# Performance work log

Measured on AMD Instinct MI355X. Metric: run time of the kernel, lower is better.

The kernel has to match this reference:

```python
import jax, jax.numpy as jnp
import numpy as np

B, N, DH, DG, HID, K_STEPS, CURV = 256, 2048, 128, 256, 256, 2, 1.0
SC = CURV ** 0.5
SCALE = 1.0 / (DH ** 0.5)
LN_EPS = 1e-5


def _artanh(x):
    return jnp.arctanh(jnp.clip(x, -1.0 + 1e-5, 1.0 - 1e-5))


def logmap0(x, sc=SC):
    n = jnp.maximum(jnp.linalg.norm(x, axis=-1, keepdims=True), 1e-7)
    return x * (_artanh(sc * n) / (sc * n))


def expmap0(v, sc=SC):
    n = jnp.maximum(jnp.linalg.norm(v, axis=-1, keepdims=True), 1e-7)
    return v * (jnp.tanh(sc * n) / (sc * n))


def setup_inputs() -> dict:
    key = jax.random.key(0)
    ks = jax.random.split(key, 16)

    def lin(k, out_d, in_d):
        return (jax.random.normal(k, (out_d, in_d), jnp.float32) * (in_d ** -0.5))

    demo_hyp = expmap0(0.1 * jax.random.normal(ks[0], (B, N, DH), jnp.float32))
    rho_g = jax.random.normal(ks[1], (B, DG), jnp.float32)
    return {
        "demo_hyp": demo_hyp,
        "rho_g": rho_g,
        "seed_g_w": lin(ks[2], DH, DG),
        "seed_g_b": jnp.zeros((DH,), jnp.float32),
        "seed_d_w": lin(ks[3], DH, DH),
        "pool_wq_w": lin(ks[4], DH, DH),
        "pool_wk_w": lin(ks[5], DH, DH),
        "pool_wv_w": lin(ks[6], DH, DH),
        "q_u_w": lin(ks[7], DH, DH),
        "q_g_w": lin(ks[8], DH, DG),
        "q_g_b": jnp.zeros((DH,), jnp.float32),
        "kv_w": lin(ks[9], DH, DH),
        "mlp_w1": lin(ks[10], HID, DH),
        "mlp_b1": jnp.zeros((HID,), jnp.float32),
        "mlp_w2": lin(ks[11], DH, HID),
        "mlp_b2": jnp.zeros((DH,), jnp.float32),
        "ln_g": jnp.ones((DH,), jnp.float32),
        "ln_b": jnp.zeros((DH,), jnp.float32),
    }


def reference(demo_hyp, rho_g, seed_g_w, seed_g_b, seed_d_w,
              pool_wq_w, pool_wk_w, pool_wv_w, q_u_w, q_g_w, q_g_b,
              kv_w, mlp_w1, mlp_b1, mlp_w2, mlp_b2, ln_g, ln_b):
    demo_tan = logmap0(demo_hyp)                       # (B,N,Dh)

    # seed: attention-pool demos with rho_g query
    q_seed = rho_g @ seed_g_w.T + seed_g_b             # (B,Dh)
    qk = q_seed @ pool_wq_w.T                          # (B,Dh)
    Kp = demo_tan @ pool_wk_w.T                        # (B,N,Dh)
    a = jax.nn.softmax(jnp.einsum('bd,bnd->bn', qk, Kp) * SCALE, axis=-1)
    Vp = demo_tan @ pool_wv_w.T
    pooled = jnp.einsum('bn,bnd->bd', a, Vp)           # (B,Dh)
    u = expmap0(q_seed + pooled @ seed_d_w.T)

    for _ in range(K_STEPS):
        u_tan = logmap0(u)
        mu = jnp.mean(u_tan, axis=-1, keepdims=True)
        var = jnp.var(u_tan, axis=-1, keepdims=True)
        u_tan = (u_tan - mu) * jax.lax.rsqrt(var + LN_EPS) * ln_g + ln_b
        q = u_tan @ q_u_w.T + rho_g @ q_g_w.T + q_g_b
        Kmat = demo_tan @ kv_w.T                       # keys == values
        att = jax.nn.softmax(jnp.einsum('bd,bnd->bn', q, Kmat) * SCALE, axis=-1)
        delta = jnp.einsum('bn,bnd->bd', att, Kmat)
        upd = jax.nn.gelu(delta @ mlp_w1.T + mlp_b1, approximate=False) @ mlp_w2.T + mlp_b2
        u = expmap0(u_tan + upd)
    return u
```

## Files before the change

kernel.cpp:

```cpp
#include <hip/hip_runtime.h>
#include <hip/hip_fp16.h>
#include <cstddef>
#include <cstdint>

#define B 256
#define N 2048
#define DH 128
#define DG 256
#define HID 256
#define WAVES 16
#define TPB (WAVES * 64)
#define RPI (WAVES * 8)
#define KIT (N / RPI)
#define SCALE 0.08838834764831845f
#define LN_EPS 1e-5f
#define TAN_NORM_MAX 6.2f


__device__ __forceinline__ float artanh_clip(float a) {
  a = fminf(a, 1.0f - 1e-5f);
  return 0.5f * __logf((1.0f + a) / (1.0f - a));
}

__device__ __forceinline__ float logmap_scale(float n2) {
  float nc = fmaxf(sqrtf(n2), 1e-7f);
  return artanh_clip(nc) / nc;
}

__device__ __forceinline__ float row16_sum(float x) {
  x += __int_as_float(__builtin_amdgcn_update_dpp(0, __float_as_int(x), 0x128, 0xF, 0xF, true));
  x += __int_as_float(__builtin_amdgcn_update_dpp(0, __float_as_int(x), 0x124, 0xF, 0xF, true));
  x += __int_as_float(__builtin_amdgcn_update_dpp(0, __float_as_int(x), 0x122, 0xF, 0xF, true));
  x += __int_as_float(__builtin_amdgcn_update_dpp(0, __float_as_int(x), 0x121, 0xF, 0xF, true));
  return x;
}

__device__ __forceinline__ float wave_allsum(float v) {
#pragma unroll
  for (int m = 1; m < 64; m <<= 1) v += __shfl_xor(v, m);
  return v;
}

__device__ __forceinline__ float dot128(const float* __restrict__ wrow,
                                        const float* __restrict__ x) {
  const float4* a = (const float4*)wrow;
  const float4* v = (const float4*)x;
  float s = 0.f;
#pragma unroll
  for (int j = 0; j < 32; ++j) {
    float4 u = a[j], b = v[j];
    s += u.x * b.x + u.y * b.y + u.z * b.z + u.w * b.w;
  }
  return s;
}

__device__ __forceinline__ float dot256(const float* __restrict__ wrow,
                                        const float* __restrict__ x) {
  const float4* a = (const float4*)wrow;
  const float4* v = (const float4*)x;
  float s = 0.f;
#pragma unroll
  for (int j = 0; j < 64; ++j) {
    float4 u = a[j], b = v[j];
    s += u.x * b.x + u.y * b.y + u.z * b.z + u.w * b.w;
  }
  return s;
}


struct __align__(16) Smem {
  float rho[DG];
  float x[DH];
  float y[DH];
  float h[HID];
  float ut[DH];
  float qseed[DH];
  float qvec[DH];
  float fold[WAVES][DH];
  float l[WAVES];
  float red[WAVES];
  float Mb;
};

__device__ __forceinline__ float bsumAll(Smem& sm, float v, int w, int lane) {
  v = wave_allsum(v);
  if (lane == 0) sm.red[w] = v;
  __syncthreads();
  float r = 0.f;
#pragma unroll
  for (int j = 0; j < WAVES; ++j) r += sm.red[j];
  __syncthreads();
  return r;
}

__device__ __forceinline__ void ln_query(Smem& sm, float v, int tid, int w, int lane,
    const float* __restrict__ q_u_w, const float* __restrict__ q_g_w,
    const float* __restrict__ q_g_b, const float* __restrict__ kv_w,
    const float* __restrict__ ln_g, const float* __restrict__ ln_b) {
  float n2 = bsumAll(sm, tid < DH ? v * v : 0.f, w, lane);
  float u = 0.f, ut = 0.f;
  if (tid < DH) {
    float nc = fmaxf(sqrtf(n2), 1e-7f);
    u = v * (tanhf(nc) / nc);
  }
  float nu2 = bsumAll(sm, tid < DH ? u * u : 0.f, w, lane);
  if (tid < DH) {
    float nuc = fmaxf(sqrtf(nu2), 1e-7f);
    ut = u * (artanh_clip(nuc) / nuc);
  }
  float mu = bsumAll(sm, tid < DH ? ut : 0.f, w, lane) * (1.0f / DH);
  float d = ut - mu;
  float var = bsumAll(sm, tid < DH ? d * d : 0.f, w, lane) * (1.0f / DH);
  if (tid < DH) {
    float y = d * rsqrtf(var + LN_EPS) * ln_g[tid] + ln_b[tid];
    sm.ut[tid] = y;
    sm.x[tid] = y;
  }
  __syncthreads();
  if (tid < DH) {
    sm.y[tid] = q_g_b[tid] + dot128(q_u_w + (size_t)tid * DH, sm.x) +
                dot256(q_g_w + (size_t)tid * DG, sm.rho);
  }
  __syncthreads();
  float qp = 0.f;
  if (tid < DH) {
#pragma unroll 8
    for (int i = 0; i < DH; ++i) qp += kv_w[i * DH + tid] * sm.y[i];
    sm.qvec[tid] = qp;
  }
  float qn2 = bsumAll(sm, tid < DH ? qp * qp : 0.f, w, lane);
  if (tid == 0) sm.Mb = SCALE * TAN_NORM_MAX * sqrtf(qn2);
  __syncthreads();
}

__device__ __forceinline__ void fold_combine(Smem& sm, float4 accL, float4 accH,
                                             float lsum, int w, int g, int il, int tid) {
  accL.x += __shfl_xor(accL.x, 16); accL.x += __shfl_xor(accL.x, 32);
  accL.y += __shfl_xor(accL.y, 16); accL.y += __shfl_xor(accL.y, 32);
  accL.z += __shfl_xor(accL.z, 16); accL.z += __shfl_xor(accL.z, 32);
  accL.w += __shfl_xor(accL.w, 16); accL.w += __shfl_xor(accL.w, 32);
  accH.x += __shfl_xor(accH.x, 16); accH.x += __shfl_xor(accH.x, 32);
  accH.y += __shfl_xor(accH.y, 16); accH.y += __shfl_xor(accH.y, 32);
  accH.z += __shfl_xor(accH.z, 16); accH.z += __shfl_xor(accH.z, 32);
  accH.w += __shfl_xor(accH.w, 16); accH.w += __shfl_xor(accH.w, 32);
  lsum += __shfl_xor(lsum, 16); lsum += __shfl_xor(lsum, 32);
  if (g == 0) {
    *(float4*)&sm.fold[w][il * 4] = accL;
    *(float4*)&sm.fold[w][64 + il * 4] = accH;
    if (il == 0) sm.l[w] = lsum;
  }
  __syncthreads();
  if (tid < DH) {
    float a = 0.f, L = 0.f;
#pragma unroll
    for (int j = 0; j < WAVES; ++j) { a += sm.fold[j][tid]; L += sm.l[j]; }
    sm.x[tid] = a / L;
  }
  __syncthreads();
}

__device__ __forceinline__ void proc_fp32(const float4 c1, const float4 c2,
    const float4 qv0, const float4 qv1, const float Mb,
    __half* __restrict__ yw,
    float& lsum, float4& accL, float4& accH) {
  float dd = qv0.x * c1.x + qv0.y * c1.y + qv0.z * c1.z + qv0.w * c1.w +
             qv1.x * c2.x + qv1.y * c2.y + qv1.z * c2.z + qv1.w * c2.w;
  float n2 = c1.x * c1.x + c1.y * c1.y + c1.z * c1.z + c1.w * c1.w +
             c2.x * c2.x + c2.y * c2.y + c2.z * c2.z + c2.w * c2.w;
  dd = row16_sum(dd);
  n2 = row16_sum(n2);
  float tsv = logmap_scale(n2);
  float4 y1 = make_float4(tsv * c1.x, tsv * c1.y, tsv * c1.z, tsv * c1.w);
  float4 y2 = make_float4(tsv * c2.x, tsv * c2.y, tsv * c2.z, tsv * c2.w);
  __half2 h01 = __float22half2_rn(make_float2(y1.x, y1.y));
  __half2 h23 = __float22half2_rn(make_float2(y1.z, y1.w));
  __half2 h45 = __float22half2_rn(make_float2(y2.x, y2.y));
  __half2 h67 = __float22half2_rn(make_float2(y2.z, y2.w));
  uint4 pk;
  pk.x = *(const unsigned*)&h01; pk.y = *(const unsigned*)&h23;
  pk.z = *(const unsigned*)&h45; pk.w = *(const unsigned*)&h67;
  *(uint4*)yw = pk;
  float pw = __expf(dd * tsv * SCALE - Mb);
  lsum += pw;
  accL.x += pw * y1.x; accL.y += pw * y1.y; accL.z += pw * y1.z; accL.w += pw * y1.w;
  accH.x += pw * y2.x; accH.y += pw * y2.y; accH.z += pw * y2.z; accH.w += pw * y2.w;
}

__device__ __forceinline__ void proc_fp16(const uint4 pk,
    const float4 qv0, const float4 qv1, const float Mb,
    float& lsum, float4& accL, float4& accH) {
  float2 f0 = __half22float2(*(const __half2*)&pk.x);
  float2 f1 = __half22float2(*(const __half2*)&pk.y);
  float2 f2 = __half22float2(*(const __half2*)&pk.z);
  float2 f3 = __half22float2(*(const __half2*)&pk.w);
  float dd = qv0.x * f0.x + qv0.y * f0.y + qv0.z * f1.x + qv0.w * f1.y +
             qv1.x * f2.x + qv1.y * f2.y + qv1.z * f3.x + qv1.w * f3.y;
  dd = row16_sum(dd);
  float pw = __expf(dd * SCALE - Mb);
  lsum += pw;
  accL.x += pw * f0.x; accL.y += pw * f0.y; accL.z += pw * f1.x; accL.w += pw * f1.y;
  accH.x += pw * f2.x; accH.y += pw * f2.y; accH.z += pw * f3.x; accH.w += pw * f3.y;
}


__global__ __launch_bounds__(TPB) void refine_a(
    const float* __restrict__ demo, const float* __restrict__ rho,
    const float* __restrict__ seed_g_w, const float* __restrict__ seed_g_b,
    const float* __restrict__ seed_d_w, const float* __restrict__ pool_wq_w,
    const float* __restrict__ pool_wk_w, const float* __restrict__ pool_wv_w,
    const float* __restrict__ q_u_w, const float* __restrict__ q_g_w,
    const float* __restrict__ q_g_b, const float* __restrict__ kv_w,
    const float* __restrict__ ln_g, const float* __restrict__ ln_b,
    __half* __restrict__ ycache, float* __restrict__ g_ut,
    float* __restrict__ g_qvec, float* __restrict__ g_mb) {
  __shared__ Smem sm;
  const int b = blockIdx.x, tid = threadIdx.x;
  const int w = tid >> 6, lane = tid & 63;
  const int g = lane >> 4, il = lane & 15;

  if (tid < DG) sm.rho[tid] = rho[(size_t)b * DG + tid];
  __syncthreads();
  if (tid < DH) {
    float qs = seed_g_b[tid] + dot256(seed_g_w + (size_t)tid * DG, sm.rho);
    sm.qseed[tid] = qs;
    sm.x[tid] = qs;
  }
  __syncthreads();
  if (tid < DH) sm.y[tid] = dot128(pool_wq_w + (size_t)tid * DH, sm.x);
  __syncthreads();
  float qp0 = 0.f;
  if (tid < DH) {
#pragma unroll 8
    for (int i = 0; i < DH; ++i) qp0 += pool_wk_w[i * DH + tid] * sm.y[i];
    sm.qvec[tid] = qp0;
  }
  float qn2 = bsumAll(sm, tid < DH ? qp0 * qp0 : 0.f, w, lane);
  if (tid == 0) sm.Mb = SCALE * TAN_NORM_MAX * sqrtf(qn2);
  __syncthreads();

  const float* p = demo + (size_t)b * N * DH + (size_t)(w * 8 + g) * DH + il * 4;
  __half* yw = ycache + (size_t)b * N * DH + (size_t)(w * 8 + g) * DH + (size_t)il * 8;
  const float4 qv0 = *(const float4*)&sm.qvec[il * 4];
  const float4 qv1 = *(const float4*)&sm.qvec[64 + il * 4];
  const float Mb = sm.Mb;

  float lsum = 0.f;
  float4 accL = make_float4(0.f, 0.f, 0.f, 0.f);
  float4 accH = make_float4(0.f, 0.f, 0.f, 0.f);

#define LD4(s1, s2, s3, s4, kk)                                   \
  do {                                                            \
    const float* pn_ = p + (size_t)(kk) * RPI * DH;               \
    s1 = *(const float4*)(pn_);                                   \
    s2 = *(const float4*)(pn_ + 64);                              \
    s3 = *(const float4*)(pn_ + 4 * DH);                          \
    s4 = *(const float4*)(pn_ + 4 * DH + 64);                     \
  } while (0)

  float4 a1A, a2A, b1A, b2A, a1B, a2B, b1B, b2B;
  LD4(a1A, a2A, b1A, b2A, 0);
  LD4(a1B, a2B, b1B, b2B, 1);

  for (int k = 0; k < KIT; k += 2) {
    {
      float4 c1 = a1A, c2 = a2A, d1 = b1A, d2 = b2A;
      if (k + 2 < KIT) LD4(a1A, a2A, b1A, b2A, k + 2);
      proc_fp32(c1, c2, qv0, qv1, Mb, yw + (size_t)k * RPI * DH, lsum, accL, accH);
      proc_fp32(d1, d2, qv0, qv1, Mb, yw + (size_t)k * RPI * DH + 4 * DH, lsum, accL, accH);
    }
    {
      float4 c1 = a1B, c2 = a2B, d1 = b1B, d2 = b2B;
      if (k + 3 < KIT) LD4(a1B, a2B, b1B, b2B, k + 3);
      proc_fp32(c1, c2, qv0, qv1, Mb, yw + (size_t)(k + 1) * RPI * DH, lsum, accL, accH);
      proc_fp32(d1, d2, qv0, qv1, Mb, yw + (size_t)(k + 1) * RPI * DH + 4 * DH, lsum, accL, accH);
    }
  }
#undef LD4

  fold_combine(sm, accL, accH, lsum, w, g, il, tid);

  if (tid < DH) sm.y[tid] = dot128(pool_wv_w + (size_t)tid * DH, sm.x);
  __syncthreads();
  float v = 0.f;
  if (tid < DH) v = sm.qseed[tid] + dot128(seed_d_w + (size_t)tid * DH, sm.y);
  ln_query(sm, v, tid, w, lane, q_u_w, q_g_w, q_g_b, kv_w, ln_g, ln_b);
  if (tid < DH) {
    g_ut[(size_t)b * DH + tid] = sm.ut[tid];
    g_qvec[(size_t)b * DH + tid] = sm.qvec[tid];
  }
  if (tid == 0) g_mb[b] = sm.Mb;
}


template <int FINAL>
__global__ __launch_bounds__(TPB) void refine_bc(
    const float* __restrict__ rho, const float* __restrict__ kv_w,
    const float* __restrict__ mlp_w1, const float* __restrict__ mlp_b1,
    const float* __restrict__ mlp_w2, const float* __restrict__ mlp_b2,
    const float* __restrict__ q_u_w, const float* __restrict__ q_g_w,
    const float* __restrict__ q_g_b, const float* __restrict__ ln_g,
    const float* __restrict__ ln_b, const __half* __restrict__ ycache,
    float* __restrict__ g_ut, float* __restrict__ g_qvec,
    float* __restrict__ g_mb, float* __restrict__ out) {
  __shared__ Smem sm;
  const int b = blockIdx.x, tid = threadIdx.x;
  const int w = tid >> 6, lane = tid & 63;
  const int g = lane >> 4, il = lane & 15;

  if (tid < DG) sm.rho[tid] = rho[(size_t)b * DG + tid];
  if (tid < DH) {
    sm.qvec[tid] = g_qvec[(size_t)b * DH + tid];
    sm.ut[tid] = g_ut[(size_t)b * DH + tid];
  }
  if (tid == 0) sm.Mb = g_mb[b];
  __syncthreads();

  const __half* yr = ycache + (size_t)b * N * DH + (size_t)(w * 8 + g) * DH + (size_t)il * 8;
  const float4 qv0 = *(const float4*)&sm.qvec[il * 4];
  const float4 qv1 = *(const float4*)&sm.qvec[64 + il * 4];
  const float Mb = sm.Mb;

  float lsum = 0.f;
  float4 accL = make_float4(0.f, 0.f, 0.f, 0.f);
  float4 accH = make_float4(0.f, 0.f, 0.f, 0.f);

#define LDY(sa, sb, kk)                                           \
  do {                                                            \
    const __half* pn_ = yr + (size_t)(kk) * RPI * DH;             \
    sa = *(const uint4*)(pn_);                                    \
    sb = *(const uint4*)(pn_ + 4 * DH);                           \
  } while (0)

  uint4 y0a, y0b, y1a, y1b, y2a, y2b, y3a, y3b;
  LDY(y0a, y0b, 0);
  LDY(y1a, y1b, 1);
  LDY(y2a, y2b, 2);
  LDY(y3a, y3b, 3);

  for (int k = 0; k < KIT; k += 4) {
    {
      uint4 pa = y0a, pb = y0b;
      if (k + 4 < KIT) LDY(y0a, y0b, k + 4);
      proc_fp16(pa, qv0, qv1, Mb, lsum, accL, accH);
      proc_fp16(pb, qv0, qv1, Mb, lsum, accL, accH);
    }
    {
      uint4 pa = y1a, pb = y1b;
      if (k + 5 < KIT) LDY(y1a, y1b, k + 5);
      proc_fp16(pa, qv0, qv1, Mb, lsum, accL, accH);
      proc_fp16(pb, qv0, qv1, Mb, lsum, accL, accH);
    }
    {
      uint4 pa = y2a, pb = y2b;
      if (k + 6 < KIT) LDY(y2a, y2b, k + 6);
      proc_fp16(pa, qv0, qv1, Mb, lsum, accL, accH);
      proc_fp16(pb, qv0, qv1, Mb, lsum, accL, accH);
    }
    {
      uint4 pa = y3a, pb = y3b;
      if (k + 7 < KIT) LDY(y3a, y3b, k + 7);
      proc_fp16(pa, qv0, qv1, Mb, lsum, accL, accH);
      proc_fp16(pb, qv0, qv1, Mb, lsum, accL, accH);
    }
  }
#undef LDY

  fold_combine(sm, accL, accH, lsum, w, g, il, tid);

  if (tid < DH) sm.y[tid] = dot128(kv_w + (size_t)tid * DH, sm.x);
  __syncthreads();
  if (tid < HID) {
    float hh = mlp_b1[tid] + dot128(mlp_w1 + (size_t)tid * DH, sm.y);
    sm.h[tid] = 0.5f * hh * (1.0f + erff(hh * 0.70710678118654752f));
  }
  __syncthreads();
  float v = 0.f;
  if (tid < DH)
    v = sm.ut[tid] + mlp_b2[tid] + dot256(mlp_w2 + (size_t)tid * HID, sm.h);
  if (FINAL) {
    float n2 = bsumAll(sm, tid < DH ? v * v : 0.f, w, lane);
    if (tid < DH) {
      float nc = fmaxf(sqrtf(n2), 1e-7f);
      out[(size_t)b * DH + tid] = v * (tanhf(nc) / nc);
    }
  } else {
    ln_query(sm, v, tid, w, lane, q_u_w, q_g_w, q_g_b, kv_w, ln_g, ln_b);
    if (tid < DH) {
      g_ut[(size_t)b * DH + tid] = sm.ut[tid];
      g_qvec[(size_t)b * DH + tid] = sm.qvec[tid];
    }
    if (tid == 0) g_mb[b] = sm.Mb;
  }
}


extern "C" void kernel_launch(void* const* d_in, const int* in_sizes, int n_in,
                              void* d_out, int out_size, void* d_ws, size_t ws_size,
                              hipStream_t stream) {
  const float* demo      = (const float*)d_in[0];
  const float* rho       = (const float*)d_in[1];
  const float* seed_g_w  = (const float*)d_in[2];
  const float* seed_g_b  = (const float*)d_in[3];
  const float* seed_d_w  = (const float*)d_in[4];
  const float* pool_wq_w = (const float*)d_in[5];
  const float* pool_wk_w = (const float*)d_in[6];
  const float* pool_wv_w = (const float*)d_in[7];
  const float* q_u_w     = (const float*)d_in[8];
  const float* q_g_w     = (const float*)d_in[9];
  const float* q_g_b     = (const float*)d_in[10];
  const float* kv_w      = (const float*)d_in[11];
  const float* mlp_w1    = (const float*)d_in[12];
  const float* mlp_b1    = (const float*)d_in[13];
  const float* mlp_w2    = (const float*)d_in[14];
  const float* mlp_b2    = (const float*)d_in[15];
  const float* ln_g      = (const float*)d_in[16];
  const float* ln_b      = (const float*)d_in[17];
  float* out = (float*)d_out;

  __half* ycache = (__half*)d_ws;
  float* fw = (float*)(ycache + (size_t)B * N * DH);
  float* g_ut   = fw;
  float* g_qvec = fw + (size_t)B * DH;
  float* g_mb   = fw + (size_t)2 * B * DH;
  (void)ws_size; (void)in_sizes; (void)n_in; (void)out_size;

  refine_a<<<B, TPB, 0, stream>>>(demo, rho, seed_g_w, seed_g_b, seed_d_w,
                                  pool_wq_w, pool_wk_w, pool_wv_w, q_u_w, q_g_w,
                                  q_g_b, kv_w, ln_g, ln_b, ycache, g_ut, g_qvec,
                                  g_mb);
  refine_bc<0><<<B, TPB, 0, stream>>>(rho, kv_w, mlp_w1, mlp_b1, mlp_w2, mlp_b2,
                                      q_u_w, q_g_w, q_g_b, ln_g, ln_b, ycache,
                                      g_ut, g_qvec, g_mb, out);
  refine_bc<1><<<B, TPB, 0, stream>>>(rho, kv_w, mlp_w1, mlp_b1, mlp_w2, mlp_b2,
                                      q_u_w, q_g_w, q_g_b, ln_g, ln_b, ycache,
                                      g_ut, g_qvec, g_mb, out);
}
```

Measured before the change: 524.2 us.

## Stage demo and fp16 key-cache streaming through LDS via async global_load_lds

Replaces the register-prefetched direct global loads in the demo pass and the fp16 cache passes with per-wave double-buffered asynchronous global-to-LDS copies. Each wave now handles 4 rows per tile, so each step covers 64 rows. Readiness is enforced with explicit s_waitcnt vmcnt counts. The aim is to keep more loads in flight without register pressure, at the cost of extra LDS traffic. It also shrinks the number of rows each wave processes per step and relies on hand-tuned vmcnt counts being correct.

```diff
diff --git a/kernel.cpp b/kernel.cpp
--- a/kernel.cpp
+++ b/kernel.cpp
@@ -10,8 +10,8 @@
 #define HID 256
 #define WAVES 16
 #define TPB (WAVES * 64)
-#define RPI (WAVES * 8)
-#define KIT (N / RPI)
+#define TROWS 64
+#define KITER (N / TROWS)
 #define SCALE 0.08838834764831845f
 #define LN_EPS 1e-5f
 #define TAN_NORM_MAX 6.2f
@@ -65,6 +65,13 @@
     s += u.x * b.x + u.y * b.y + u.z * b.z + u.w * b.w;
   }
   return s;
+}
+
+
+typedef __attribute__((address_space(3))) void lds_vp;
+typedef __attribute__((address_space(1))) const void gm_vp;
+__device__ __forceinline__ void dma16(const void* g, void* l) {
+  __builtin_amdgcn_global_load_lds((gm_vp*)g, (lds_vp*)l, 16, 0, 0);
 }
 
 
@@ -214,6 +221,7 @@
     __half* __restrict__ ycache, float* __restrict__ g_ut,
     float* __restrict__ g_qvec, float* __restrict__ g_mb) {
   __shared__ Smem sm;
+  __shared__ __align__(16) char stg[WAVES * 2 * 2048];
   const int b = blockIdx.x, tid = threadIdx.x;
   const int w = tid >> 6, lane = tid & 63;
   const int g = lane >> 4, il = lane & 15;
@@ -238,44 +246,41 @@
   if (tid == 0) sm.Mb = SCALE * TAN_NORM_MAX * sqrtf(qn2);
   __syncthreads();
 
-  const float* p = demo + (size_t)b * N * DH + (size_t)(w * 8 + g) * DH + il * 4;
-  __half* yw = ycache + (size_t)b * N * DH + (size_t)(w * 8 + g) * DH + (size_t)il * 8;
+  const float* demo_b = demo + (size_t)b * N * DH;
   const float4 qv0 = *(const float4*)&sm.qvec[il * 4];
   const float4 qv1 = *(const float4*)&sm.qvec[64 + il * 4];
   const float Mb = sm.Mb;
+  __half* yw = ycache + (size_t)b * N * DH + (size_t)(w * 4 + g) * DH + (size_t)il * 8;
+
+  char* mybuf = stg + (size_t)w * 4096;
+  const char* gsrc0 = (const char*)demo_b + (size_t)(w * 4) * 512 + (size_t)lane * 16;
 
   float lsum = 0.f;
   float4 accL = make_float4(0.f, 0.f, 0.f, 0.f);
   float4 accH = make_float4(0.f, 0.f, 0.f, 0.f);
 
-#define LD4(s1, s2, s3, s4, kk)                                   \
-  do {                                                            \
-    const float* pn_ = p + (size_t)(kk) * RPI * DH;               \
-    s1 = *(const float4*)(pn_);                                   \
-    s2 = *(const float4*)(pn_ + 64);                              \
-    s3 = *(const float4*)(pn_ + 4 * DH);                          \
-    s4 = *(const float4*)(pn_ + 4 * DH + 64);                     \
-  } while (0)
-
-  float4 a1A, a2A, b1A, b2A, a1B, a2B, b1B, b2B;
-  LD4(a1A, a2A, b1A, b2A, 0);
-  LD4(a1B, a2B, b1B, b2B, 1);
-
-  for (int k = 0; k < KIT; k += 2) {
-    {
-      float4 c1 = a1A, c2 = a2A, d1 = b1A, d2 = b2A;
-      if (k + 2 < KIT) LD4(a1A, a2A, b1A, b2A, k + 2);
-      proc_fp32(c1, c2, qv0, qv1, Mb, yw + (size_t)k * RPI * DH, lsum, accL, accH);
-      proc_fp32(d1, d2, qv0, qv1, Mb, yw + (size_t)k * RPI * DH + 4 * DH, lsum, accL, accH);
-    }
-    {
-      float4 c1 = a1B, c2 = a2B, d1 = b1B, d2 = b2B;
-      if (k + 3 < KIT) LD4(a1B, a2B, b1B, b2B, k + 3);
-      proc_fp32(c1, c2, qv0, qv1, Mb, yw + (size_t)(k + 1) * RPI * DH, lsum, accL, accH);
-      proc_fp32(d1, d2, qv0, qv1, Mb, yw + (size_t)(k + 1) * RPI * DH + 4 * DH, lsum, accL, accH);
-    }
-  }
-#undef LD4
+  auto stage32 = [&](int t, int sel) {
+    const char* s = gsrc0 + (size_t)t * (TROWS * 512);
+    char* d = mybuf + sel * 2048;
+    dma16(s, d);
+    dma16(s + 1024, d + 1024);
+  };
+  auto proc_tile32 = [&](int sel, int t) {
+    const float* lb = (const float*)(mybuf + sel * 2048);
+    float4 c1 = *(const float4*)(lb + g * 128 + il * 4);
+    float4 c2 = *(const float4*)(lb + g * 128 + 64 + il * 4);
+    proc_fp32(c1, c2, qv0, qv1, Mb, yw + (size_t)t * TROWS * DH, lsum, accL, accH);
+  };
+
+  stage32(0, 0);
+  stage32(1, 1);
+  asm volatile("s_waitcnt vmcnt(2)" ::: "memory");
+  proc_tile32(0, 0);
+  for (int k = 1; k < KITER; ++k) {
+    stage32(k + 1 < KITER ? k + 1 : 0, (k + 1) & 1);
+    asm volatile("s_waitcnt vmcnt(3)" ::: "memory");
+    proc_tile32(k & 1, k);
+  }
 
   fold_combine(sm, accL, accH, lsum, w, g, il, tid);
 
@@ -303,6 +308,7 @@
     float* __restrict__ g_ut, float* __restrict__ g_qvec,
     float* __restrict__ g_mb, float* __restrict__ out) {
   __shared__ Smem sm;
+  __shared__ __align__(16) char stg[WAVES * 2 * 1024];
   const int b = blockIdx.x, tid = threadIdx.x;
   const int w = tid >> 6, lane = tid & 63;
   const int g = lane >> 4, il = lane & 15;
@@ -315,55 +321,33 @@
   if (tid == 0) sm.Mb = g_mb[b];
   __syncthreads();
 
-  const __half* yr = ycache + (size_t)b * N * DH + (size_t)(w * 8 + g) * DH + (size_t)il * 8;
+  const __half* yc_b = ycache + (size_t)b * N * DH;
   const float4 qv0 = *(const float4*)&sm.qvec[il * 4];
   const float4 qv1 = *(const float4*)&sm.qvec[64 + il * 4];
   const float Mb = sm.Mb;
 
+  char* mybuf = stg + (size_t)w * 2048;
+  const char* gsrc0 = (const char*)yc_b + (size_t)(w * 4) * 256 + (size_t)lane * 16;
+
   float lsum = 0.f;
   float4 accL = make_float4(0.f, 0.f, 0.f, 0.f);
   float4 accH = make_float4(0.f, 0.f, 0.f, 0.f);
 
-#define LDY(sa, sb, kk)                                           \
-  do {                                                            \
-    const __half* pn_ = yr + (size_t)(kk) * RPI * DH;             \
-    sa = *(const uint4*)(pn_);                                    \
-    sb = *(const uint4*)(pn_ + 4 * DH);                           \
-  } while (0)
-
-  uint4 y0a, y0b, y1a, y1b, y2a, y2b, y3a, y3b;
-  LDY(y0a, y0b, 0);
-  LDY(y1a, y1b, 1);
-  LDY(y2a, y2b, 2);
-  LDY(y3a, y3b, 3);
-
-  for (int k = 0; k < KIT; k += 4) {
-    {
-      uint4 pa = y0a, pb = y0b;
-      if (k + 4 < KIT) LDY(y0a, y0b, k + 4);
-      proc_fp16(pa, qv0, qv1, Mb, lsum, accL, accH);
-      proc_fp16(pb, qv0, qv1, Mb, lsum, accL, accH);
-    }
-    {
-      uint4 pa = y1a, pb = y1b;
-      if (k + 5 < KIT) LDY(y1a, y1b, k + 5);
-      proc_fp16(pa, qv0, qv1, Mb, lsum, accL, accH);
-      proc_fp16(pb, qv0, qv1, Mb, lsum, accL, accH);
-    }
-    {
-      uint4 pa = y2a, pb = y2b;
-      if (k + 6 < KIT) LDY(y2a, y2b, k + 6);
-      proc_fp16(pa, qv0, qv1, Mb, lsum, accL, accH);
-      proc_fp16(pb, qv0, qv1, Mb, lsum, accL, accH);
-    }
-    {
-      uint4 pa = y3a, pb = y3b;
-      if (k + 7 < KIT) LDY(y3a, y3b, k + 7);
-      proc_fp16(pa, qv0, qv1, Mb, lsum, accL, accH);
-      proc_fp16(pb, qv0, qv1, Mb, lsum, accL, accH);
-    }
-  }
-#undef LDY
+  auto stage16 = [&](int t, int sel) {
+    dma16(gsrc0 + (size_t)t * (TROWS * 256), mybuf + sel * 1024);
+  };
+  auto proc_tile16 = [&](int sel) {
+    const char* lb = mybuf + sel * 1024;
+    uint4 pk = *(const uint4*)(lb + g * 256 + il * 16);
+    proc_fp16(pk, qv0, qv1, Mb, lsum, accL, accH);
+  };
+
+  stage16(0, 0);
+  for (int k = 0; k < KITER; ++k) {
+    stage16(k + 1 < KITER ? k + 1 : 0, (k + 1) & 1);
+    asm volatile("s_waitcnt vmcnt(1)" ::: "memory");
+    proc_tile16(k & 1);
+  }
 
   fold_combine(sm, accL, accH, lsum, w, g, il, tid);
 
```

New measurement: 519.2 us. No clear change (-1.0%).
